# Kernel tuning notes

Measured on AMD Instinct MI355X. Metric: run time of the kernel, lower is better.

## Reference

```python
import jax, jax.numpy as jnp
import numpy as np

NUM_HEADS = 16

def setup_inputs() -> dict:
    key = jax.random.key(0)
    k1, k2, k3 = jax.random.split(key, 3)
    B, S, D = 2, 2048, 1024
    return {
        "hidden_states": jax.random.normal(k1, (B, S, D), dtype=jnp.float32),
        "W_attn": jax.random.normal(k2, (D, 3 * D), dtype=jnp.float32) * 0.02,
        "b_attn": jnp.zeros((3 * D,), dtype=jnp.float32),
        "W_proj": jax.random.normal(k3, (D, D), dtype=jnp.float32) * 0.02,
        "b_proj": jnp.zeros((D,), dtype=jnp.float32),
    }

def reference(hidden_states, W_attn, b_attn, W_proj, b_proj):
    B, S, D = hidden_states.shape
    H = NUM_HEADS
    hd = D // H
    # qkv projection (Conv1D == addmm): [B,S,3D]
    qkv = hidden_states @ W_attn + b_attn
    q, k, v = jnp.split(qkv, 3, axis=-1)
    # split heads -> [B,H,S,hd]
    def split_heads(t):
        return t.reshape(B, S, H, hd).transpose(0, 2, 1, 3)
    q, k, v = split_heads(q), split_heads(k), split_heads(v)
    # scaled QK^T: [B,H,S,S]
    scores = jnp.einsum('bhqd,bhkd->bhqk', q, k) / jnp.asarray(hd ** 0.5, dtype=q.dtype)
    causal = jnp.tril(jnp.ones((S, S), dtype=bool))
    mask_value = jnp.finfo(scores.dtype).min
    scores = jnp.where(causal, scores, mask_value)
    probs = jax.nn.softmax(scores, axis=-1)  # attn_pdrop=0 -> no dropout
    out = jnp.einsum('bhqk,bhkd->bhqd', probs, v)
    # merge heads -> [B,S,D]
    out = out.transpose(0, 2, 1, 3).reshape(B, S, D)
    out = out @ W_proj + b_proj  # resid_pdrop=0 -> no dropout
    return out
```

## Files before the change

### kernel.cpp

```cpp
#include <hip/hip_runtime.h>
#include <math.h>

typedef __attribute__((ext_vector_type(8))) short bf16x8;
typedef __attribute__((ext_vector_type(4))) short bf16x4;
typedef __attribute__((ext_vector_type(4))) float f32x4;

#define MFMA16(a, b, c) __builtin_amdgcn_mfma_f32_16x16x32_bf16(a, b, c, 0, 0, 0)

#define GLOAD_LDS16(g, l)                                                        \
    __builtin_amdgcn_global_load_lds(                                            \
        (const __attribute__((address_space(1))) void*)(g),                      \
        (__attribute__((address_space(3))) void*)(l), 16, 0, 0)

#define SBAR() __builtin_amdgcn_s_barrier()
#define PRIO(x) __builtin_amdgcn_s_setprio(x)
#define VMW6 asm volatile("s_waitcnt vmcnt(6)" ::: "memory")
#define VMW4 asm volatile("s_waitcnt vmcnt(4)" ::: "memory")
#define VMW2 asm volatile("s_waitcnt vmcnt(2)" ::: "memory")
#define VMW0 asm volatile("s_waitcnt vmcnt(0)" ::: "memory")
#define NOPS ((void)0)

__device__ __forceinline__ short f2bf(float f) {
    union { float f; unsigned u; } x; x.f = f;
    unsigned r = (x.u + 0x7fffu + ((x.u >> 16) & 1u)) >> 16;
    return (short)r;
}

__global__ __launch_bounds__(256) void prep_kernel(
    const float* __restrict__ hs, short* __restrict__ hs_bf,
    const float* __restrict__ Wa, const float* __restrict__ Wp,
    short* __restrict__ WaT, short* __restrict__ WpT) {
    __shared__ float tile[32][33];
    const int bid = blockIdx.x;
    if (bid < 4096) {
        int i = bid * 256 + threadIdx.x;
        float4 v = ((const float4*)hs)[i];
        bf16x4 o;
        o[0] = f2bf(v.x); o[1] = f2bf(v.y); o[2] = f2bf(v.z); o[3] = f2bf(v.w);
        ((bf16x4*)hs_bf)[i] = o;
        return;
    }
    const int xb2 = bid - 4096;
    const int xbb = xb2 & 127;
    const int ky = xb2 >> 7;
    const float* W; short* Wt; int N, xb;
    if (xbb < 96) { W = Wa; Wt = WaT; N = 3072; xb = xbb; }
    else          { W = Wp; Wt = WpT; N = 1024; xb = xbb - 96; }
    const int K = 1024;
    int c = threadIdx.x & 31, r0 = threadIdx.x >> 5;
    int n0 = xb << 5, k0 = ky << 5;
#pragma unroll
    for (int i = 0; i < 4; i++) {
        int r = r0 + i * 8;
        tile[r][c] = W[(long)(k0 + r) * N + n0 + c];
    }
    __syncthreads();
#pragma unroll
    for (int i = 0; i < 4; i++) {
        int r = r0 + i * 8;
        Wt[(long)(n0 + r) * K + k0 + c] = f2bf(tile[c][r]);
    }
}

#define LDA8(IDX) (*(const bf16x8*)&ls[(IDX)])
#define SA(q, k1v, nbv) GLOAD_LDS16(Ags + (size_t)(q) * 65536 + (k1v), &ls[(nbv) + (q) * 4096 + swd])
#define SB(q, k1v, nbv) GLOAD_LDS16(Bgs + (size_t)(q) * 65536 + (k1v), &ls[(nbv) + 32768 + (q) * 4096 + swd])

#define PHASE_MFMA(M0_, M1_, aa0, ba0, aa1, ba1)              \
    PRIO(1);                                                  \
    acc[M0_][0] = MFMA16(aa0, b00, acc[M0_][0]);              \
    acc[M0_][1] = MFMA16(aa0, b10, acc[M0_][1]);              \
    acc[M0_][2] = MFMA16(aa0, b20, acc[M0_][2]);              \
    acc[M0_][3] = MFMA16(aa0, b30, acc[M0_][3]);              \
    acc[M1_][0] = MFMA16(ba0, b00, acc[M1_][0]);              \
    acc[M1_][1] = MFMA16(ba0, b10, acc[M1_][1]);              \
    acc[M1_][2] = MFMA16(ba0, b20, acc[M1_][2]);              \
    acc[M1_][3] = MFMA16(ba0, b30, acc[M1_][3]);              \
    acc[M0_][0] = MFMA16(aa1, b01, acc[M0_][0]);              \
    acc[M0_][1] = MFMA16(aa1, b11, acc[M0_][1]);              \
    acc[M0_][2] = MFMA16(aa1, b21, acc[M0_][2]);              \
    acc[M0_][3] = MFMA16(aa1, b31, acc[M0_][3]);              \
    acc[M1_][0] = MFMA16(ba1, b01, acc[M1_][0]);              \
    acc[M1_][1] = MFMA16(ba1, b11, acc[M1_][1]);              \
    acc[M1_][2] = MFMA16(ba1, b21, acc[M1_][2]);              \
    acc[M1_][3] = MFMA16(ba1, b31, acc[M1_][3]);              \
    PRIO(0);

#define KTILE(T, STG, VMP2, VMTAIL) do {                                              \
    const int cb = ((T) & 1) << 14;                                                   \
    const int nb = cb ^ 16384;                                                        \
    const int k1 = ((T) + 1) << 6;                                                    \
    (void)nb; (void)k1;                                                               \
                                                                    \
    if (STG) { SB(0, k1, nb); SB(1, k1, nb); }                                        \
    const bf16x8 b00 = LDA8(cb + 32768 + bro + sw0);                                  \
    const bf16x8 b01 = LDA8(cb + 32768 + bro + sw1);                                  \
    const bf16x8 b10 = LDA8(cb + 32768 + bro + 1024 + sw0);                           \
    const bf16x8 b11 = LDA8(cb + 32768 + bro + 1024 + sw1);                           \
    const bf16x8 b20 = LDA8(cb + 32768 + bro + 2048 + sw0);                           \
    const bf16x8 b21 = LDA8(cb + 32768 + bro + 2048 + sw1);                           \
    const bf16x8 b30 = LDA8(cb + 32768 + bro + 3072 + sw0);                           \
    const bf16x8 b31 = LDA8(cb + 32768 + bro + 3072 + sw1);                           \
    {                                                                                 \
        bf16x8 x0 = LDA8(cb + aro + sw0), x1 = LDA8(cb + aro + sw1);                  \
        bf16x8 y0 = LDA8(cb + aro + 1024 + sw0), y1 = LDA8(cb + aro + 1024 + sw1);    \
        SBAR();                                                                       \
        PHASE_MFMA(0, 1, x0, y0, x1, y1)                                              \
        SBAR();                                                                       \
    }                                                                                 \
                                                                    \
    if (STG) { SB(2, k1, nb); SB(3, k1, nb); }                                        \
    {                                                                                 \
        bf16x8 x0 = LDA8(cb + aro + 2048 + sw0), x1 = LDA8(cb + aro + 2048 + sw1);    \
        bf16x8 y0 = LDA8(cb + aro + 3072 + sw0), y1 = LDA8(cb + aro + 3072 + sw1);    \
        SBAR();                                                                       \
        PHASE_MFMA(2, 3, x0, y0, x1, y1)                                              \
        SBAR();                                                                       \
    }                                                                                 \
                                                                    \
    VMP2;                                                                             \
    SBAR();                                                                           \
    if (STG) { SA(0, k1, nb); SA(2, k1, nb); }                                        \
    {                                                                                 \
        bf16x8 x0 = LDA8(cb + aro + 4096 + sw0), x1 = LDA8(cb + aro + 4096 + sw1);    \
        bf16x8 y0 = LDA8(cb + aro + 5120 + sw0), y1 = LDA8(cb + aro + 5120 + sw1);    \
        PHASE_MFMA(4, 5, x0, y0, x1, y1)                                              \
        SBAR();                                                                       \
    }                                                                                 \
                                                                    \
    if (STG) { SA(1, k1, nb); SA(3, k1, nb); }                                        \
    {                                                                                 \
        bf16x8 x0 = LDA8(cb + aro + 6144 + sw0), x1 = LDA8(cb + aro + 6144 + sw1);    \
        bf16x8 y0 = LDA8(cb + aro + 7168 + sw0), y1 = LDA8(cb + aro + 7168 + sw1);    \
        SBAR();                                                                       \
        PHASE_MFMA(6, 7, x0, y0, x1, y1)                                              \
        VMTAIL;                                                                       \
        SBAR();                                                                       \
    }                                                                                 \
} while (0)

__global__ __launch_bounds__(512, 2) void gemm_qkv_kernel(
    const short* __restrict__ A, const short* __restrict__ Bt,
    const float* __restrict__ bias,
    short* __restrict__ QK, short* __restrict__ VTb) {
    __shared__ __align__(16) short ls[65536];
    const int tid = threadIdx.x;
    const int lane = tid & 63, l15 = lane & 15, quad = lane >> 4;
    const int w = tid >> 6, wm = w >> 2, wn = w & 3;
    const int m0 = blockIdx.y * 256, n0 = blockIdx.x * 256;
    const int e = l15 & 7;
    const int sgr = (w << 3) + (lane >> 3);
    const int sgc = ((lane & 7) ^ (lane >> 3)) << 3;
    const int swd = w << 9;
    const short* Ags = A + (size_t)(m0 + sgr) * 1024 + sgc;
    const short* Bgs = Bt + (size_t)(n0 + sgr) * 1024 + sgc;
    const int aro = (wm * 128 + l15) << 6;
    const int bro = (wn * 64 + l15) << 6;
    const int sw0 = (quad ^ e) << 3;
    const int sw1 = ((4 + quad) ^ e) << 3;

    f32x4 acc[8][4];
#pragma unroll
    for (int i = 0; i < 8; i++)
#pragma unroll
        for (int j = 0; j < 4; j++) acc[i][j] = (f32x4){0.f, 0.f, 0.f, 0.f};

    SB(0, 0, 0); SB(1, 0, 0); SB(2, 0, 0); SB(3, 0, 0);
    SA(0, 0, 0); SA(2, 0, 0); SA(1, 0, 0); SA(3, 0, 0);
    VMW2;
    SBAR();

#pragma unroll 2
    for (int t = 0; t < 14; ++t) { KTILE(t, 1, VMW4, VMW2); }
    KTILE(14, 1, VMW4, VMW0);
    KTILE(15, 0, VMW0, NOPS);

    __syncthreads();

    if (n0 < 2048) {
        const float scale = (n0 < 1024) ? 0.18033688011112042f : 1.0f;
        short* qt_ = &ls[w * 4352];
        const int colbase = n0 + wn * 64;
        const int rrow = lane >> 3;
        const int rcol = (lane & 7) << 3;
#pragma unroll
        for (int half = 0; half < 2; half++) {
#pragma unroll
            for (int nt = 0; nt < 4; nt++) {
                const int nn = colbase + nt * 16 + l15;
                const float bv = bias[nn];
#pragma unroll
                for (int mt = 0; mt < 4; mt++) {
                    const int mtg = half * 4 + mt;
#pragma unroll
                    for (int r = 0; r < 4; r++)
                        qt_[(mt * 16 + quad * 4 + r) * 68 + nt * 16 + l15] =
                            f2bf((acc[mtg][nt][r] + bv) * scale);
                }
            }
#pragma unroll
            for (int i = 0; i < 8; i++) {
                const int mrow = i * 8 + rrow;
                bf16x8 vv = *(const bf16x8*)&qt_[mrow * 68 + rcol];
                const int mm = m0 + wm * 128 + half * 64 + mrow;
                *(bf16x8*)&QK[(size_t)mm * 2048 + colbase + rcol] = vv;
            }
        }
    } else {
        short* vt = &ls[w * 4352];
        const int hh = ((n0 - 2048) >> 6) + wn;
        const int bb = m0 >> 11;
        const int srow = (m0 & 2047) + wm * 128;
        const int sloc = (lane & 7) << 3;
#pragma unroll
        for (int half = 0; half < 2; half++) {
#pragma unroll
            for (int nt = 0; nt < 4; nt++) {
                const int nn = n0 + wn * 64 + nt * 16 + l15;
                const float bv = bias[nn];
                const int d_ = nt * 16 + l15;
#pragma unroll
                for (int mt = 0; mt < 4; mt++) {
                    const int mtg = half * 4 + mt;
                    bf16x4 pk;
#pragma unroll
                    for (int r = 0; r < 4; r++) pk[r] = f2bf(acc[mtg][nt][r] + bv);
                    *(bf16x4*)&vt[d_ * 68 + mt * 16 + quad * 4] = pk;
                }
            }
#pragma unroll
            for (int i = 0; i < 8; i++) {
                const int d = i * 8 + (lane >> 3);
                bf16x8 vv = *(const bf16x8*)&vt[d * 68 + sloc];
                *(bf16x8*)&VTb[((size_t)(bb * 16 + hh) * 64 + d) * 2048 + srow + half * 64 + sloc] = vv;
            }
        }
    }
}

#define PJ_ISSUE(K0, BB) do {                                                               \
    const int i0 = (w << 2);                                                                \
    GLOAD_LDS16(&Ap[(size_t)((i0 << 3) + lrow) * 1024 + (K0) + lgcol], &ls[(BB) + i0 * 512]);             \
    GLOAD_LDS16(&Ap[(size_t)(((i0 + 1) << 3) + lrow) * 1024 + (K0) + lgcol], &ls[(BB) + (i0 + 1) * 512]); \
    GLOAD_LDS16(&Ap[(size_t)(((i0 + 2) << 3) + lrow) * 1024 + (K0) + lgcol], &ls[(BB) + (i0 + 2) * 512]); \
    GLOAD_LDS16(&Ap[(size_t)(((i0 + 3) << 3) + lrow) * 1024 + (K0) + lgcol], &ls[(BB) + (i0 + 3) * 512]); \
    const int j0 = (w << 1);                                                                \
    GLOAD_LDS16(&Bp[(size_t)((j0 << 3) + lrow) * 1024 + (K0) + lgcol], &ls[(BB) + 8192 + j0 * 512]);      \
    GLOAD_LDS16(&Bp[(size_t)(((j0 + 1) << 3) + lrow) * 1024 + (K0) + lgcol], &ls[(BB) + 8192 + (j0 + 1) * 512]); \
} while (0)

__global__ __launch_bounds__(256, 2) void gemm_proj_kernel(
    const short* __restrict__ A, const short* __restrict__ Bt,
    const float* __restrict__ bias, float* __restrict__ outF) {
    __shared__ __align__(16) short ls[36864];
    const int tid = threadIdx.x;
    const int lane = tid & 63, l15 = lane & 15, quad = lane >> 4, w = tid >> 6;
    const int bid = blockIdx.x;
    const int wk = (bid & 7) * 64 + (bid >> 3);
    const int m0 = (wk >> 4) * 128, n0 = (wk & 15) * 64;
    const int e = l15 & 7;
    const int lrow = lane >> 3;
    const int lgcol = ((lane & 7) ^ lrow) << 3;
    const short* Ap = A + (size_t)m0 * 1024;
    const short* Bp = Bt + (size_t)n0 * 1024;

    f32x4 acc[2][4];
#pragma unroll
    for (int i = 0; i < 2; i++)
#pragma unroll
        for (int j = 0; j < 4; j++) acc[i][j] = (f32x4){0.f, 0.f, 0.f, 0.f};

    PJ_ISSUE(0, 0);
    PJ_ISSUE(64, 12288);
    VMW6;
    SBAR();

    int cur = 0;
    for (int t = 0; t < 16; ++t) {
        const int bb = cur * 12288;
        if (t < 14) {
            const int nb2 = (cur == 0) ? 24576 : (cur - 1) * 12288;
            PJ_ISSUE((t + 2) << 6, nb2);
        }
#pragma unroll
        for (int kb = 0; kb < 8; kb += 4) {
            const int sw = (((kb + quad) ^ e) << 3);
            bf16x8 af0 = *(const bf16x8*)&ls[bb + (w * 32 + l15) * 64 + sw];
            bf16x8 af1 = *(const bf16x8*)&ls[bb + (w * 32 + 16 + l15) * 64 + sw];
            bf16x8 bf0 = *(const bf16x8*)&ls[bb + 8192 + (l15) * 64 + sw];
            bf16x8 bf1 = *(const bf16x8*)&ls[bb + 8192 + (16 + l15) * 64 + sw];
            bf16x8 bf2 = *(const bf16x8*)&ls[bb + 8192 + (32 + l15) * 64 + sw];
            bf16x8 bf3 = *(const bf16x8*)&ls[bb + 8192 + (48 + l15) * 64 + sw];
            PRIO(1);
            acc[0][0] = MFMA16(af0, bf0, acc[0][0]);
            acc[0][1] = MFMA16(af0, bf1, acc[0][1]);
            acc[0][2] = MFMA16(af0, bf2, acc[0][2]);
            acc[0][3] = MFMA16(af0, bf3, acc[0][3]);
            acc[1][0] = MFMA16(af1, bf0, acc[1][0]);
            acc[1][1] = MFMA16(af1, bf1, acc[1][1]);
            acc[1][2] = MFMA16(af1, bf2, acc[1][2]);
            acc[1][3] = MFMA16(af1, bf3, acc[1][3]);
            PRIO(0);
        }
        if (t < 14) { VMW6; SBAR(); }
        else if (t == 14) { VMW0; SBAR(); }
        cur = (cur == 2) ? 0 : cur + 1;
    }

#pragma unroll
    for (int nt = 0; nt < 4; nt++) {
        int nn = n0 + nt * 16 + l15;
        float bv = bias[nn];
#pragma unroll
        for (int mt = 0; mt < 2; mt++)
#pragma unroll
            for (int r = 0; r < 4; r++) {
                int mm = m0 + w * 32 + mt * 16 + quad * 4 + r;
                outF[(long)mm * 1024 + nn] = acc[mt][nt][r] + bv;
            }
    }
}

__global__ __launch_bounds__(512, 4) void attn_kernel(
    const short* __restrict__ QK, const short* __restrict__ VT,
    short* __restrict__ Ao) {
    __shared__ __align__(16) short Kt[2][128 * 64];
    __shared__ __align__(16) short Vt[2][2][64 * 64];
    __shared__ __align__(16) short Pt[8][1024];
    const int tid = threadIdx.x;
    const int lane = tid & 63, l15 = lane & 15, quad = lane >> 4, w = tid >> 6;
    const int bx = blockIdx.x;
    const int u = bx >> 5;
    const int qt = (u < 8) ? u : (23 - u);
    const int hb = bx & 31;
    const int b = hb >> 4, h = hb & 15;
    const size_t rowbase = (size_t)b * 2048 * 2048 + h * 64;
    const short* Qb = QK + rowbase;
    const short* Kb = QK + rowbase + 1024;
    const short* Vh = VT + (size_t)hb * 64 * 2048;
    short* Pw = &Pt[w][0];
    const int e = l15 & 7;

    const int srow0 = tid >> 3;
    const int sc4 = (tid & 7) ^ (srow0 & 7);
    const int wdst = w << 9;

    const long qr = (long)(qt * 128 + w * 16 + l15) * 2048;
    bf16x8 qf0 = *(const bf16x8*)&Qb[qr + quad * 8];
    bf16x8 qf1 = *(const bf16x8*)&Qb[qr + 32 + quad * 8];

    float l = 0.f;
    f32x4 o[4];
#pragma unroll
    for (int dt = 0; dt < 4; dt++) o[dt] = (f32x4){0.f, 0.f, 0.f, 0.f};

    const int nc = qt + 1;

    const short* kp = Kb + (size_t)srow0 * 2048 + sc4 * 8;
    const short* vp = Vh + (size_t)srow0 * 2048 + sc4 * 8;

    GLOAD_LDS16(kp, &Kt[0][wdst]);
    GLOAD_LDS16(kp + 64 * 2048, &Kt[0][4096 + wdst]);
    GLOAD_LDS16(vp, &Vt[0][0][wdst]);
    GLOAD_LDS16(vp + 64, &Vt[0][1][wdst]);
    VMW0;
    SBAR();

    for (int c = 0; c < nc; c++) {
        const short* Kc = &Kt[c & 1][0];
        if (c + 1 < nc) {
            kp += 128 * 2048;
            vp += 128;
            const int nb = (c + 1) & 1;
            GLOAD_LDS16(kp, &Kt[nb][wdst]);
            GLOAD_LDS16(kp + 64 * 2048, &Kt[nb][4096 + wdst]);
            GLOAD_LDS16(vp, &Vt[nb][0][wdst]);
            GLOAD_LDS16(vp + 64, &Vt[nb][1][wdst]);
        }
        const bool diag = (c == nc - 1);

#pragma unroll
        for (int half = 0; half < 2; half++) {
            const short* Kh = Kc + half * 4096;
            const short* Vc = &Vt[c & 1][half][0];

            f32x4 s[4];
#pragma unroll
            for (int t = 0; t < 4; t++) {
                bf16x8 k0f = *(const bf16x8*)&Kh[(t * 16 + l15) * 64 + ((quad ^ e) << 3)];
                bf16x8 k1f = *(const bf16x8*)&Kh[(t * 16 + l15) * 64 + (((4 + quad) ^ e) << 3)];
                f32x4 z = (f32x4){0.f, 0.f, 0.f, 0.f};
                z = MFMA16(k0f, qf0, z);
                z = MFMA16(k1f, qf1, z);
                s[t] = z;
            }

            if (diag) {
#pragma unroll
                for (int t = 0; t < 4; t++)
#pragma unroll
                    for (int r = 0; r < 4; r++)
                        if (half * 64 + t * 16 + quad * 4 + r > w * 16 + l15)
                            s[t][r] = -INFINITY;
            }

#pragma unroll
            for (int t = 0; t < 4; t++) {
                bf16x4 pw;
#pragma unroll
                for (int r = 0; r < 4; r++) {
                    float pv = __builtin_amdgcn_exp2f(s[t][r]);
                    l += pv;
                    pw[r] = f2bf(pv);
                }
                *(bf16x4*)&Pw[l15 * 64 + (((2 * t + (quad >> 1)) ^ e) << 3) + ((quad & 1) << 2)] = pw;
            }

            bf16x8 pf0 = *(const bf16x8*)&Pw[l15 * 64 + ((quad ^ e) << 3)];
            bf16x8 pf1 = *(const bf16x8*)&Pw[l15 * 64 + (((4 + quad) ^ e) << 3)];
#pragma unroll
            for (int dt = 0; dt < 4; dt++) {
                bf16x8 v0f = *(const bf16x8*)&Vc[(dt * 16 + l15) * 64 + ((quad ^ e) << 3)];
                bf16x8 v1f = *(const bf16x8*)&Vc[(dt * 16 + l15) * 64 + (((4 + quad) ^ e) << 3)];
                o[dt] = MFMA16(v0f, pf0, o[dt]);
                o[dt] = MFMA16(v1f, pf1, o[dt]);
            }
        }

        VMW0;
        SBAR();
    }

    l += __shfl_xor(l, 16);
    l += __shfl_xor(l, 32);
    const float rl = 1.f / l;

    const int qs = qt * 128 + w * 16 + l15;
    const long base = ((long)(b * 2048 + qs)) * 1024 + h * 64;
#pragma unroll
    for (int dt = 0; dt < 4; dt++) {
        bf16x4 wv;
#pragma unroll
        for (int r = 0; r < 4; r++) wv[r] = f2bf(o[dt][r] * rl);
        *(bf16x4*)&Ao[base + dt * 16 + quad * 4] = wv;
    }
}

extern "C" void kernel_launch(void* const* d_in, const int* in_sizes, int n_in,
                              void* d_out, int out_size, void* d_ws, size_t ws_size,
                              hipStream_t stream) {
    const float* hs = (const float*)d_in[0];
    const float* W_attn = (const float*)d_in[1];
    const float* b_attn = (const float*)d_in[2];
    const float* W_proj = (const float*)d_in[3];
    const float* b_proj = (const float*)d_in[4];
    float* out = (float*)d_out;

    const size_t MB = 1024 * 1024;
    char* ws = (char*)d_ws;
    short* hs_bf = (short*)ws;
    short* attn_o = hs_bf;
    short* WaT = (short*)(ws + 8 * MB);
    short* WpT = (short*)(ws + 14 * MB);
    short* QK = (short*)(ws + 16 * MB);
    short* VTb = (short*)(ws + 32 * MB);

    prep_kernel<<<8192, 256, 0, stream>>>(hs, hs_bf, W_attn, W_proj, WaT, WpT);
    gemm_qkv_kernel<<<dim3(12, 16), 512, 0, stream>>>(hs_bf, WaT, b_attn, QK, VTb);
    attn_kernel<<<512, 512, 0, stream>>>(QK, VTb, attn_o);
    gemm_proj_kernel<<<512, 256, 0, stream>>>(attn_o, WpT, b_proj, out);
}
```

Before: 164.4 us.

## Have each attention wave process two 16-row query tiles with 256-thread blocks

The attention block drops from 8 waves to 4, and each wave now handles 32 query rows as two 16-row MFMA tiles that share the same K and V fragments read from LDS. This halves the LDS reads of K/V per query row and gives each wave more independent MFMA chains. In exchange, each thread issues twice as many global-to-LDS loads, registers per thread roughly double, and launch bounds change to 256 threads with 2 blocks. The block count stays the same, so fewer waves are resident per CU.

```diff
diff --git a/kernel.cpp b/kernel.cpp
--- a/kernel.cpp
+++ b/kernel.cpp
@@ -321,12 +321,12 @@
     }
 }
 
-__global__ __launch_bounds__(512, 4) void attn_kernel(
+__global__ __launch_bounds__(256, 2) void attn_kernel(
     const short* __restrict__ QK, const short* __restrict__ VT,
     short* __restrict__ Ao) {
     __shared__ __align__(16) short Kt[2][128 * 64];
     __shared__ __align__(16) short Vt[2][2][64 * 64];
-    __shared__ __align__(16) short Pt[8][1024];
+    __shared__ __align__(16) short Pt[4][2][1024];
     const int tid = threadIdx.x;
     const int lane = tid & 63, l15 = lane & 15, quad = lane >> 4, w = tid >> 6;
     const int bx = blockIdx.x;
@@ -338,21 +338,28 @@
     const short* Qb = QK + rowbase;
     const short* Kb = QK + rowbase + 1024;
     const short* Vh = VT + (size_t)hb * 64 * 2048;
-    short* Pw = &Pt[w][0];
+    short* Pw0 = &Pt[w][0][0];
+    short* Pw1 = &Pt[w][1][0];
     const int e = l15 & 7;
 
     const int srow0 = tid >> 3;
     const int sc4 = (tid & 7) ^ (srow0 & 7);
     const int wdst = w << 9;
 
-    const long qr = (long)(qt * 128 + w * 16 + l15) * 2048;
-    bf16x8 qf0 = *(const bf16x8*)&Qb[qr + quad * 8];
-    bf16x8 qf1 = *(const bf16x8*)&Qb[qr + 32 + quad * 8];
-
-    float l = 0.f;
-    f32x4 o[4];
-#pragma unroll
-    for (int dt = 0; dt < 4; dt++) o[dt] = (f32x4){0.f, 0.f, 0.f, 0.f};
+    const long qr0 = (long)(qt * 128 + w * 32 + l15) * 2048;
+    const long qr1 = qr0 + 16 * 2048;
+    bf16x8 qf00 = *(const bf16x8*)&Qb[qr0 + quad * 8];
+    bf16x8 qf01 = *(const bf16x8*)&Qb[qr0 + 32 + quad * 8];
+    bf16x8 qf10 = *(const bf16x8*)&Qb[qr1 + quad * 8];
+    bf16x8 qf11 = *(const bf16x8*)&Qb[qr1 + 32 + quad * 8];
+
+    float l0 = 0.f, l1 = 0.f;
+    f32x4 o0[4], o1[4];
+#pragma unroll
+    for (int dt = 0; dt < 4; dt++) {
+        o0[dt] = (f32x4){0.f, 0.f, 0.f, 0.f};
+        o1[dt] = (f32x4){0.f, 0.f, 0.f, 0.f};
+    }
 
     const int nc = qt + 1;
 
@@ -360,9 +367,13 @@
     const short* vp = Vh + (size_t)srow0 * 2048 + sc4 * 8;
 
     GLOAD_LDS16(kp, &Kt[0][wdst]);
+    GLOAD_LDS16(kp + 32 * 2048, &Kt[0][2048 + wdst]);
     GLOAD_LDS16(kp + 64 * 2048, &Kt[0][4096 + wdst]);
+    GLOAD_LDS16(kp + 96 * 2048, &Kt[0][6144 + wdst]);
     GLOAD_LDS16(vp, &Vt[0][0][wdst]);
+    GLOAD_LDS16(vp + 32 * 2048, &Vt[0][0][2048 + wdst]);
     GLOAD_LDS16(vp + 64, &Vt[0][1][wdst]);
+    GLOAD_LDS16(vp + 32 * 2048 + 64, &Vt[0][1][2048 + wdst]);
     VMW0;
     SBAR();
 
@@ -373,9 +384,13 @@
             vp += 128;
             const int nb = (c + 1) & 1;
             GLOAD_LDS16(kp, &Kt[nb][wdst]);
+            GLOAD_LDS16(kp + 32 * 2048, &Kt[nb][2048 + wdst]);
             GLOAD_LDS16(kp + 64 * 2048, &Kt[nb][4096 + wdst]);
+            GLOAD_LDS16(kp + 96 * 2048, &Kt[nb][6144 + wdst]);
             GLOAD_LDS16(vp, &Vt[nb][0][wdst]);
+            GLOAD_LDS16(vp + 32 * 2048, &Vt[nb][0][2048 + wdst]);
             GLOAD_LDS16(vp + 64, &Vt[nb][1][wdst]);
+            GLOAD_LDS16(vp + 32 * 2048 + 64, &Vt[nb][1][2048 + wdst]);
         }
         const bool diag = (c == nc - 1);
 
@@ -384,46 +399,60 @@
             const short* Kh = Kc + half * 4096;
             const short* Vc = &Vt[c & 1][half][0];
 
-            f32x4 s[4];
+            f32x4 s0[4], s1[4];
 #pragma unroll
             for (int t = 0; t < 4; t++) {
                 bf16x8 k0f = *(const bf16x8*)&Kh[(t * 16 + l15) * 64 + ((quad ^ e) << 3)];
                 bf16x8 k1f = *(const bf16x8*)&Kh[(t * 16 + l15) * 64 + (((4 + quad) ^ e) << 3)];
-                f32x4 z = (f32x4){0.f, 0.f, 0.f, 0.f};
-                z = MFMA16(k0f, qf0, z);
-                z = MFMA16(k1f, qf1, z);
-                s[t] = z;
+                f32x4 z0 = (f32x4){0.f, 0.f, 0.f, 0.f};
+                z0 = MFMA16(k0f, qf00, z0);
+                z0 = MFMA16(k1f, qf01, z0);
+                s0[t] = z0;
+                f32x4 z1 = (f32x4){0.f, 0.f, 0.f, 0.f};
+                z1 = MFMA16(k0f, qf10, z1);
+                z1 = MFMA16(k1f, qf11, z1);
+                s1[t] = z1;
             }
 
             if (diag) {
+                const int lq0 = w * 32 + l15, lq1 = lq0 + 16;
 #pragma unroll
                 for (int t = 0; t < 4; t++)
 #pragma unroll
-                    for (int r = 0; r < 4; r++)
-                        if (half * 64 + t * 16 + quad * 4 + r > w * 16 + l15)
-                            s[t][r] = -INFINITY;
+                    for (int r = 0; r < 4; r++) {
+                        const int kk = half * 64 + t * 16 + quad * 4 + r;
+                        if (kk > lq0) s0[t][r] = -INFINITY;
+                        if (kk > lq1) s1[t][r] = -INFINITY;
+                    }
             }
 
 #pragma unroll
             for (int t = 0; t < 4; t++) {
-                bf16x4 pw;
+                bf16x4 pw0, pw1;
 #pragma unroll
                 for (int r = 0; r < 4; r++) {
-                    float pv = __builtin_amdgcn_exp2f(s[t][r]);
-                    l += pv;
-                    pw[r] = f2bf(pv);
+                    float p0 = __builtin_amdgcn_exp2f(s0[t][r]);
+                    float p1 = __builtin_amdgcn_exp2f(s1[t][r]);
+                    l0 += p0; l1 += p1;
+                    pw0[r] = f2bf(p0); pw1[r] = f2bf(p1);
                 }
-                *(bf16x4*)&Pw[l15 * 64 + (((2 * t + (quad >> 1)) ^ e) << 3) + ((quad & 1) << 2)] = pw;
-            }
-
-            bf16x8 pf0 = *(const bf16x8*)&Pw[l15 * 64 + ((quad ^ e) << 3)];
-            bf16x8 pf1 = *(const bf16x8*)&Pw[l15 * 64 + (((4 + quad) ^ e) << 3)];
+                const int poff = l15 * 64 + (((2 * t + (quad >> 1)) ^ e) << 3) + ((quad & 1) << 2);
+                *(bf16x4*)&Pw0[poff] = pw0;
+                *(bf16x4*)&Pw1[poff] = pw1;
+            }
+
+            bf16x8 pf00 = *(const bf16x8*)&Pw0[l15 * 64 + ((quad ^ e) << 3)];
+            bf16x8 pf01 = *(const bf16x8*)&Pw0[l15 * 64 + (((4 + quad) ^ e) << 3)];
+            bf16x8 pf10 = *(const bf16x8*)&Pw1[l15 * 64 + ((quad ^ e) << 3)];
+            bf16x8 pf11 = *(const bf16x8*)&Pw1[l15 * 64 + (((4 + quad) ^ e) << 3)];
 #pragma unroll
             for (int dt = 0; dt < 4; dt++) {
                 bf16x8 v0f = *(const bf16x8*)&Vc[(dt * 16 + l15) * 64 + ((quad ^ e) << 3)];
                 bf16x8 v1f = *(const bf16x8*)&Vc[(dt * 16 + l15) * 64 + (((4 + quad) ^ e) << 3)];
-                o[dt] = MFMA16(v0f, pf0, o[dt]);
-                o[dt] = MFMA16(v1f, pf1, o[dt]);
+                o0[dt] = MFMA16(v0f, pf00, o0[dt]);
+                o0[dt] = MFMA16(v1f, pf01, o0[dt]);
+                o1[dt] = MFMA16(v0f, pf10, o1[dt]);
+                o1[dt] = MFMA16(v1f, pf11, o1[dt]);
             }
         }
 
@@ -431,18 +460,26 @@
         SBAR();
     }
 
-    l += __shfl_xor(l, 16);
-    l += __shfl_xor(l, 32);
-    const float rl = 1.f / l;
-
-    const int qs = qt * 128 + w * 16 + l15;
-    const long base = ((long)(b * 2048 + qs)) * 1024 + h * 64;
+    l0 += __shfl_xor(l0, 16);
+    l0 += __shfl_xor(l0, 32);
+    l1 += __shfl_xor(l1, 16);
+    l1 += __shfl_xor(l1, 32);
+    const float rl0 = 1.f / l0;
+    const float rl1 = 1.f / l1;
+
+    const int qs0 = qt * 128 + w * 32 + l15;
+    const long base0 = ((long)(b * 2048 + qs0)) * 1024 + h * 64;
+    const long base1 = base0 + 16 * 1024;
 #pragma unroll
     for (int dt = 0; dt < 4; dt++) {
-        bf16x4 wv;
-#pragma unroll
-        for (int r = 0; r < 4; r++) wv[r] = f2bf(o[dt][r] * rl);
-        *(bf16x4*)&Ao[base + dt * 16 + quad * 4] = wv;
+        bf16x4 wv0, wv1;
+#pragma unroll
+        for (int r = 0; r < 4; r++) {
+            wv0[r] = f2bf(o0[dt][r] * rl0);
+            wv1[r] = f2bf(o1[dt][r] * rl1);
+        }
+        *(bf16x4*)&Ao[base0 + dt * 16 + quad * 4] = wv0;
+        *(bf16x4*)&Ao[base1 + dt * 16 + quad * 4] = wv1;
     }
 }
 
@@ -467,6 +504,6 @@
 
     prep_kernel<<<8192, 256, 0, stream>>>(hs, hs_bf, W_attn, W_proj, WaT, WpT);
     gemm_qkv_kernel<<<dim3(12, 16), 512, 0, stream>>>(hs_bf, WaT, b_attn, QK, VTb);
-    attn_kernel<<<512, 512, 0, stream>>>(QK, VTb, attn_o);
+    attn_kernel<<<512, 256, 0, stream>>>(QK, VTb, attn_o);
     gemm_proj_kernel<<<512, 256, 0, stream>>>(attn_o, WpT, b_proj, out);
 }
```

After: 169.0 us. 1.03x slower.
